# Optimization experiments

Hardware: AMD Instinct MI355X
Metric: run time of the kernel (lower is better)

## Reference

```python
import jax, jax.numpy as jnp
import numpy as np

N_NODES = 100000
N_EDGES = 500000
HEADS = 4
HID = 64
N_GRAPHS = 512
EPS_SM = 1e-8
EPS_BN = 1e-5


def setup_inputs() -> dict:
    key = jax.random.key(0)
    ks = jax.random.split(key, 8)
    x = jax.random.normal(ks[0], (N_NODES, HID), dtype=jnp.float32)
    edge_index = jax.random.randint(ks[1], (2, N_EDGES), 0, N_NODES, dtype=jnp.int64)
    batch = jnp.sort(jax.random.randint(ks[2], (N_NODES,), 0, N_GRAPHS, dtype=jnp.int64))
    Ws = jax.random.normal(ks[3], (3, HEADS * HID, HID), dtype=jnp.float32) * 0.08
    att_src = jax.random.normal(ks[4], (3, HEADS, HID), dtype=jnp.float32) * 0.1
    att_dst = jax.random.normal(ks[5], (3, HEADS, HID), dtype=jnp.float32) * 0.1
    bn_gamma = jnp.ones((2, HID), dtype=jnp.float32)
    bn_beta = jnp.zeros((2, HID), dtype=jnp.float32)
    bn_mean = jnp.zeros((2, HID), dtype=jnp.float32)
    bn_var = jnp.ones((2, HID), dtype=jnp.float32)
    fc_w = jax.random.normal(ks[6], (2, HID), dtype=jnp.float32) * 0.1
    fc_b = jnp.zeros((2,), dtype=jnp.float32)
    return {"x": x, "edge_index": edge_index, "batch": batch, "Ws": Ws,
            "att_src": att_src, "att_dst": att_dst, "bn_gamma": bn_gamma,
            "bn_beta": bn_beta, "bn_mean": bn_mean, "bn_var": bn_var,
            "fc_w": fc_w, "fc_b": fc_b}


def gat_layer(x, row, col, W, a_src, a_dst):
    # x: [N, F] -> h: [N, H, C]
    n = x.shape[0]
    h = (x @ W.T).reshape(n, HEADS, HID)
    a_s = jnp.sum(h * a_src[None], axis=-1)          # [N, H]
    a_d = jnp.sum(h * a_dst[None], axis=-1)          # [N, H]
    e = a_s[row] + a_d[col]                          # [E, H]
    e = jnp.where(e >= 0, e, 0.2 * e)                # LeakyReLU(0.2)
    # segment softmax over destination node (col)
    e_max = jax.ops.segment_max(e, col, num_segments=n)  # [N, H]
    p = jnp.exp(e - e_max[col])
    p_sum = jax.ops.segment_sum(p, col, num_segments=n)
    alpha = p / (p_sum[col] + EPS_SM)                # [E, H]
    msg = h[row] * alpha[:, :, None]                 # [E, H, C]
    out = jax.ops.segment_sum(msg, col, num_segments=n)  # [N, H, C]
    return out.mean(axis=1)                          # [N, C]


def reference(x, edge_index, batch, Ws, att_src, att_dst,
              bn_gamma, bn_beta, bn_mean, bn_var, fc_w, fc_b):
    row, col = edge_index[0], edge_index[1]
    h = x
    for i in range(2):  # first num_layers-1 layers: conv -> BN(eval) -> ReLU
        h = gat_layer(h, row, col, Ws[i], att_src[i], att_dst[i])
        h = (h - bn_mean[i]) * jax.lax.rsqrt(bn_var[i] + EPS_BN) * bn_gamma[i] + bn_beta[i]
        h = jax.nn.relu(h)
        # dropout is inactive in eval mode
    h = gat_layer(h, row, col, Ws[2], att_src[2], att_dst[2])
    # global mean pool over graphs in batch
    sums = jax.ops.segment_sum(h, batch, num_segments=N_GRAPHS)          # [G, C]
    cnts = jax.ops.segment_sum(jnp.ones_like(batch, dtype=h.dtype), batch,
                               num_segments=N_GRAPHS)                    # [G]
    pooled = sums / jnp.maximum(cnts, 1.0)[:, None]
    return pooled @ fc_w.T + fc_b                                        # [G, out]
```

## Files before the change

### kernel.cpp

```cpp
#include <hip/hip_runtime.h>


#define THREADS 256
#define LDP 36

__global__ __launch_bounds__(THREADS) void k_prep(
    const float* __restrict__ Ws, const float* __restrict__ att_src,
    const float* __restrict__ att_dst, float* __restrict__ fold)
{
    int idx = blockIdx.x * THREADS + threadIdx.x;
    if (idx >= 3 * 2 * 4 * 64) return;
    int k = idx & 63, head = (idx >> 6) & 3, sd = (idx >> 8) & 1, l = idx >> 9;
    const float* att = (sd ? att_dst : att_src) + l * 256 + head * 64;
    const float* Wb  = Ws + (size_t)l * 16384 + (size_t)head * 64 * 64;
    float s = 0.f;
    #pragma unroll
    for (int c = 0; c < 64; ++c) s = fmaf(Wb[(size_t)c * 64 + k], att[c], s);
    fold[((l * 2 + sd) * 4 + head) * 64 + k] = s;
}

__global__ __launch_bounds__(THREADS) void k_gemm(
    const float* __restrict__ x, const float* __restrict__ W,
    float* __restrict__ h, int n)
{
    __shared__ float xs[128][LDP];
    __shared__ float ws[128][LDP];
    const int tid  = threadIdx.x;
    const int tc   = tid & 15;
    const int tr   = tid >> 4;
    const int row0 = blockIdx.x * 128;
    const int col0 = blockIdx.y * 128;

    float acc[8][8];
    #pragma unroll
    for (int i = 0; i < 8; ++i)
        #pragma unroll
        for (int j = 0; j < 8; ++j) acc[i][j] = 0.f;

    for (int ks2 = 0; ks2 < 2; ++ks2) {
        #pragma unroll
        for (int i = 0; i < 4; ++i) {
            int flat4 = i * 256 + tid;
            int r  = flat4 >> 3;
            int c4 = flat4 & 7;
            int gr = row0 + r;
            float4 v = make_float4(0.f, 0.f, 0.f, 0.f);
            if (gr < n) v = *(const float4*)(x + (size_t)gr * 64 + ks2 * 32 + c4 * 4);
            *(float4*)&xs[r][c4 * 4] = v;
            int gp = col0 + r;
            int pr = (gp & 3) * 64 + (gp >> 2);
            float4 wv = *(const float4*)(W + (size_t)pr * 64 + ks2 * 32 + c4 * 4);
            *(float4*)&ws[r][c4 * 4] = wv;
        }
        __syncthreads();

        #pragma unroll 1
        for (int ks = 0; ks < 8; ++ks) {
            float4 xr[8];
            #pragma unroll
            for (int i = 0; i < 8; ++i) xr[i] = *(const float4*)&xs[tr + 16 * i][ks * 4];
            #pragma unroll
            for (int j = 0; j < 8; ++j) {
                float4 w4 = *(const float4*)&ws[tc + 16 * j][ks * 4];
                #pragma unroll
                for (int i = 0; i < 8; ++i) {
                    acc[i][j] = fmaf(xr[i].x, w4.x, acc[i][j]);
                    acc[i][j] = fmaf(xr[i].y, w4.y, acc[i][j]);
                    acc[i][j] = fmaf(xr[i].z, w4.z, acc[i][j]);
                    acc[i][j] = fmaf(xr[i].w, w4.w, acc[i][j]);
                }
            }
        }
        __syncthreads();
    }

    #pragma unroll
    for (int i = 0; i < 8; ++i) {
        int r = row0 + tr + 16 * i;
        if (r < n) {
            float* hp = h + (size_t)r * 256 + col0 + tc;
            #pragma unroll
            for (int j = 0; j < 8; ++j) hp[16 * j] = acc[i][j];
        }
    }
}

__global__ __launch_bounds__(THREADS) void k_att(
    const float* __restrict__ x, const float* __restrict__ fold_l,
    float* __restrict__ a_s, float* __restrict__ a_d, int n)
{
    int wid  = (blockIdx.x * THREADS + threadIdx.x) >> 6;
    int lane = threadIdx.x & 63;
    if (wid >= n) return;
    int vec = lane >> 3, ch = lane & 7;
    const float* xp = x + (size_t)wid * 64 + ch * 8;
    float4 v0 = *(const float4*)xp;
    float4 v1 = *(const float4*)(xp + 4);
    const float* fp = fold_l + vec * 64 + ch * 8;
    float acc = v0.x * fp[0] + v0.y * fp[1] + v0.z * fp[2] + v0.w * fp[3]
              + v1.x * fp[4] + v1.y * fp[5] + v1.z * fp[6] + v1.w * fp[7];
    acc += __shfl_xor(acc, 1, 64);
    acc += __shfl_xor(acc, 2, 64);
    acc += __shfl_xor(acc, 4, 64);
    if (ch == 0) {
        if (vec < 4) a_s[(size_t)wid * 4 + vec] = acc;
        else         a_d[(size_t)wid * 4 + (vec - 4)] = acc;
    }
}

__global__ __launch_bounds__(THREADS) void k_hist(
    const int* __restrict__ col, int* __restrict__ hist, int E)
{
    int e = blockIdx.x * THREADS + threadIdx.x;
    if (e < E) atomicAdd(hist + col[e], 1);
}

__global__ __launch_bounds__(THREADS) void k_scan1(
    const int* __restrict__ hist, int* __restrict__ offs, int* __restrict__ partials, int n)
{
    __shared__ int buf0[256], buf1[256];
    int tid = threadIdx.x;
    int i = blockIdx.x * 256 + tid;
    int v = (i < n) ? hist[i] : 0;
    buf0[tid] = v;
    __syncthreads();
    int* src = buf0; int* dst = buf1;
    #pragma unroll
    for (int off = 1; off < 256; off <<= 1) {
        int t = src[tid];
        if (tid >= off) t += src[tid - off];
        dst[tid] = t;
        __syncthreads();
        int* tmp = src; src = dst; dst = tmp;
    }
    if (i < n) offs[i] = src[tid] - v;
    if (tid == 255) partials[blockIdx.x] = src[255];
}

__global__ __launch_bounds__(512) void k_scan2(int* __restrict__ partials, int nb)
{
    __shared__ int buf0[512], buf1[512];
    int tid = threadIdx.x;
    int v = (tid < nb) ? partials[tid] : 0;
    buf0[tid] = v;
    __syncthreads();
    int* src = buf0; int* dst = buf1;
    #pragma unroll
    for (int off = 1; off < 512; off <<= 1) {
        int t = src[tid];
        if (tid >= off) t += src[tid - off];
        dst[tid] = t;
        __syncthreads();
        int* tmp = src; src = dst; dst = tmp;
    }
    if (tid < nb) partials[tid] = src[tid] - v;
}

__global__ __launch_bounds__(THREADS) void k_scan3(
    int* __restrict__ offs, const int* __restrict__ partials, int n)
{
    int i = blockIdx.x * THREADS + threadIdx.x;
    if (i < n) offs[i] += partials[i >> 8];
}

__global__ __launch_bounds__(THREADS) void k_scatter(
    const int* __restrict__ row, const int* __restrict__ col,
    const int* __restrict__ offs, int* __restrict__ tmpc,
    int* __restrict__ rs, int E)
{
    int e = blockIdx.x * THREADS + threadIdx.x;
    if (e >= E) return;
    int c = col[e];
    int pos = offs[c] + atomicAdd(tmpc + c, 1);
    rs[pos] = row[e];
}

__global__ __launch_bounds__(THREADS) void k_alpha(
    const int* __restrict__ rs, const int* __restrict__ offs, const int* __restrict__ deg,
    const float* __restrict__ a_s, const float* __restrict__ a_d,
    float* __restrict__ alpha, float* __restrict__ psum, int n)
{
    int v = blockIdx.x * THREADS + threadIdx.x;
    if (v >= n) return;
    const int start = offs[v];
    const int d     = deg[v];
    const float4 ad = *(const float4*)(a_d + (size_t)v * 4);

    float m0 = -1e30f, m1 = -1e30f, m2 = -1e30f, m3 = -1e30f;
    for (int i = 0; i < d; ++i) {
        int r = rs[start + i];
        float4 as = *(const float4*)(a_s + (size_t)r * 4);
        float v0 = as.x + ad.x, v1 = as.y + ad.y, v2 = as.z + ad.z, v3 = as.w + ad.w;
        v0 = v0 >= 0.f ? v0 : 0.2f * v0;
        v1 = v1 >= 0.f ? v1 : 0.2f * v1;
        v2 = v2 >= 0.f ? v2 : 0.2f * v2;
        v3 = v3 >= 0.f ? v3 : 0.2f * v3;
        *(float4*)(alpha + (size_t)(start + i) * 4) = make_float4(v0, v1, v2, v3);
        m0 = fmaxf(m0, v0); m1 = fmaxf(m1, v1); m2 = fmaxf(m2, v2); m3 = fmaxf(m3, v3);
    }
    float ps0 = 0.f, ps1 = 0.f, ps2 = 0.f, ps3 = 0.f;
    for (int i = 0; i < d; ++i) {
        float4 s = *(const float4*)(alpha + (size_t)(start + i) * 4);
        float p0 = __expf(s.x - m0), p1 = __expf(s.y - m1);
        float p2 = __expf(s.z - m2), p3 = __expf(s.w - m3);
        ps0 += p0; ps1 += p1; ps2 += p2; ps3 += p3;
        *(float4*)(alpha + (size_t)(start + i) * 4) = make_float4(p0, p1, p2, p3);
    }
    *(float4*)(psum + (size_t)v * 4) = make_float4(ps0, ps1, ps2, ps3);
}

__global__ __launch_bounds__(THREADS) void k_gat(
    const int* __restrict__ rs, const int* __restrict__ offs, const int* __restrict__ deg,
    const float* __restrict__ alpha, const float* __restrict__ psum,
    const float* __restrict__ h,
    const float* __restrict__ bng, const float* __restrict__ bnb,
    const float* __restrict__ bnm, const float* __restrict__ bnv, int use_bn,
    float* __restrict__ out, int n)
{
    int wid  = (blockIdx.x * THREADS + threadIdx.x) >> 6;
    int lane = threadIdx.x & 63;
    if (wid >= n) return;
    const int start = offs[wid];
    const int d     = deg[wid];
    float4 ps = *(const float4*)(psum + (size_t)wid * 4);
    const float i0 = 0.25f / (ps.x + 1e-8f), i1 = 0.25f / (ps.y + 1e-8f);
    const float i2 = 0.25f / (ps.z + 1e-8f), i3 = 0.25f / (ps.w + 1e-8f);

    float acc = 0.f;
    for (int i = 0; i < d; ++i) {
        int r = rs[start + i];
        float4 a = *(const float4*)(alpha + (size_t)(start + i) * 4);
        float4 v = *(const float4*)(h + (size_t)r * 256 + lane * 4);
        acc = fmaf(a.x * i0, v.x, acc);
        acc = fmaf(a.y * i1, v.y, acc);
        acc = fmaf(a.z * i2, v.z, acc);
        acc = fmaf(a.w * i3, v.w, acc);
    }
    if (use_bn) {
        float scale = bng[lane] * rsqrtf(bnv[lane] + 1e-5f);
        float shift = bnb[lane] - bnm[lane] * scale;
        acc = fmaxf(fmaf(acc, scale, shift), 0.f);
    }
    out[(size_t)wid * 64 + lane] = acc;
}

#define POOL_CHUNK 32
__global__ __launch_bounds__(THREADS) void k_pool(
    const float* __restrict__ xf, const int* __restrict__ batch,
    float* __restrict__ sums, float* __restrict__ cnt, int n)
{
    int wid  = (blockIdx.x * THREADS + threadIdx.x) >> 6;
    int lane = threadIdx.x & 63;
    int n0 = wid * POOL_CHUNK;
    if (n0 >= n) return;
    int n1 = min(n0 + POOL_CHUNK, n);
    int g = batch[n0];
    float acc = 0.f, c = 0.f;
    for (int i = n0; i < n1; ++i) {
        int gi = batch[i];
        if (gi != g) {
            atomicAdd(sums + (size_t)g * 64 + lane, acc);
            if (lane == 0) atomicAdd(cnt + g, c);
            g = gi; acc = 0.f; c = 0.f;
        }
        acc += xf[(size_t)i * 64 + lane];
        c += 1.f;
    }
    atomicAdd(sums + (size_t)g * 64 + lane, acc);
    if (lane == 0) atomicAdd(cnt + g, c);
}

__global__ __launch_bounds__(THREADS) void k_fc(
    const float* __restrict__ sums, const float* __restrict__ cnt,
    const float* __restrict__ fw, const float* __restrict__ fb,
    float* __restrict__ out, int G)
{
    int g = blockIdx.x * THREADS + threadIdx.x;
    if (g >= G) return;
    float cdiv = fmaxf(cnt[g], 1.f);
    float o0 = fb[0], o1 = fb[1];
    for (int k = 0; k < 64; ++k) {
        float p = sums[(size_t)g * 64 + k] / cdiv;
        o0 = fmaf(p, fw[k], o0);
        o1 = fmaf(p, fw[64 + k], o1);
    }
    out[(size_t)g * 2 + 0] = o0;
    out[(size_t)g * 2 + 1] = o1;
}

static inline size_t align256(size_t x) { return (x + 255) & ~(size_t)255; }

extern "C" void kernel_launch(void* const* d_in, const int* in_sizes, int n_in,
                              void* d_out, int out_size, void* d_ws, size_t ws_size,
                              hipStream_t stream)
{
    const float* x        = (const float*)d_in[0];
    const int*   eidx     = (const int*)d_in[1];
    const int*   batch    = (const int*)d_in[2];
    const float* Ws       = (const float*)d_in[3];
    const float* att_src  = (const float*)d_in[4];
    const float* att_dst  = (const float*)d_in[5];
    const float* bn_gamma = (const float*)d_in[6];
    const float* bn_beta  = (const float*)d_in[7];
    const float* bn_mean  = (const float*)d_in[8];
    const float* bn_var   = (const float*)d_in[9];
    const float* fc_w     = (const float*)d_in[10];
    const float* fc_b     = (const float*)d_in[11];

    const int N = in_sizes[0] / 64;
    const int E = in_sizes[1] / 2;
    const int G = 512;
    const int* row = eidx;
    const int* col = eidx + E;

    char* p = (char*)d_ws;
    float* h     = (float*)p; p += align256((size_t)N * 256 * 4);
    float* a_s   = (float*)p; p += align256((size_t)N * 4 * 4);
    float* a_d   = (float*)p; p += align256((size_t)N * 4 * 4);
    float* psum  = (float*)p; p += align256((size_t)N * 4 * 4);
    float* xb0   = (float*)p; p += align256((size_t)N * 64 * 4);
    float* xb1   = (float*)p; p += align256((size_t)N * 64 * 4);
    int*   hist  = (int*)p;   p += align256((size_t)N * 4);
    int*   offs  = (int*)p;   p += align256((size_t)N * 4);
    int*   tmpc  = (int*)p;   p += align256((size_t)N * 4);
    int*   part  = (int*)p;   p += align256((size_t)1024 * 4);
    int*   rs    = (int*)p;   p += align256((size_t)E * 4);
    float* alpha = (float*)p; p += align256((size_t)E * 4 * 4);
    float* fold  = (float*)p; p += align256((size_t)1536 * 4);
    float* sums  = (float*)p; p += align256((size_t)G * 64 * 4);
    float* cnt   = (float*)p; p += align256((size_t)G * 4);
    (void)ws_size; (void)n_in; (void)out_size;

    const int nb = (N + 255) / 256;

    k_prep<<<6, THREADS, 0, stream>>>(Ws, att_src, att_dst, fold);
    hipMemsetAsync(hist, 0, (size_t)N * 4, stream);
    hipMemsetAsync(tmpc, 0, (size_t)N * 4, stream);
    k_hist<<<(E + THREADS - 1) / THREADS, THREADS, 0, stream>>>(col, hist, E);
    k_scan1<<<nb, THREADS, 0, stream>>>(hist, offs, part, N);
    k_scan2<<<1, 512, 0, stream>>>(part, nb);
    k_scan3<<<nb, THREADS, 0, stream>>>(offs, part, N);
    k_scatter<<<(E + THREADS - 1) / THREADS, THREADS, 0, stream>>>(row, col, offs, tmpc, rs, E);

    const float* xin = x;
    for (int l = 0; l < 3; ++l) {
        float* xout = (l == 1) ? xb1 : xb0;
        dim3 ggrid((N + 127) / 128, 2);
        k_gemm<<<ggrid, THREADS, 0, stream>>>(xin, Ws + (size_t)l * 16384, h, N);
        k_att<<<((size_t)N * 64 + THREADS - 1) / THREADS, THREADS, 0, stream>>>(
            xin, fold + (size_t)l * 512, a_s, a_d, N);
        k_alpha<<<(N + THREADS - 1) / THREADS, THREADS, 0, stream>>>(
            rs, offs, hist, a_s, a_d, alpha, psum, N);
        k_gat<<<((size_t)N * 64 + THREADS - 1) / THREADS, THREADS, 0, stream>>>(
            rs, offs, hist, alpha, psum, h,
            bn_gamma + l * 64, bn_beta + l * 64, bn_mean + l * 64, bn_var + l * 64,
            (l < 2) ? 1 : 0, xout, N);
        xin = xout;
    }

    hipMemsetAsync(sums, 0, (size_t)G * 64 * 4, stream);
    hipMemsetAsync(cnt, 0, (size_t)G * 4, stream);
    int pool_waves = (N + POOL_CHUNK - 1) / POOL_CHUNK;
    k_pool<<<((size_t)pool_waves * 64 + THREADS - 1) / THREADS, THREADS, 0, stream>>>(
        xin, batch, sums, cnt, N);
    k_fc<<<(G + THREADS - 1) / THREADS, THREADS, 0, stream>>>(
        sums, cnt, fc_w, fc_b, (float*)d_out, G);
}
```

Baseline: 611.2 us.

## Fuse attention logits into GEMM and parallelize segment softmax per edge

Attention score projections a_s and a_d are now computed inside the GEMM kernel's y=0 blocks from the already staged shared-memory x tile, which removes the separate k_att pass. The per-node serial softmax kernel is replaced by two edge-parallel kernels. One computes the LeakyReLU scores and takes the per-node max with order-preserving unsigned atomicMax. The other exponentiates and accumulates psum with float atomicAdd. This trades the load imbalance of the thread-per-node loop for atomic contention, extra index arrays (dsb, pose), and per-layer memsets.

```diff
diff --git a/kernel.cpp b/kernel.cpp
--- a/kernel.cpp
+++ b/kernel.cpp
@@ -3,6 +3,15 @@
 
 #define THREADS 256
 #define LDP 36
+#define SFP 68
+
+__device__ __forceinline__ unsigned fkey(float f) {
+    unsigned u = __float_as_uint(f);
+    return (u & 0x80000000u) ? ~u : (u | 0x80000000u);
+}
+__device__ __forceinline__ float funkey(unsigned u) {
+    return __uint_as_float((u & 0x80000000u) ? (u & 0x7FFFFFFFu) : ~u);
+}
 
 __global__ __launch_bounds__(THREADS) void k_prep(
     const float* __restrict__ Ws, const float* __restrict__ att_src,
@@ -21,21 +30,33 @@
 
 __global__ __launch_bounds__(THREADS) void k_gemm(
     const float* __restrict__ x, const float* __restrict__ W,
-    float* __restrict__ h, int n)
+    const float* __restrict__ fold_l,
+    float* __restrict__ h, float* __restrict__ a_s, float* __restrict__ a_d, int n)
 {
     __shared__ float xs[128][LDP];
     __shared__ float ws[128][LDP];
+    __shared__ float sf[8 * SFP];
     const int tid  = threadIdx.x;
     const int tc   = tid & 15;
     const int tr   = tid >> 4;
     const int row0 = blockIdx.x * 128;
     const int col0 = blockIdx.y * 128;
+    const bool gy0 = (blockIdx.y == 0);
+
+    if (gy0) {
+        #pragma unroll
+        for (int j = 0; j < 2; ++j) {
+            int idx = j * 256 + tid;
+            sf[(idx >> 6) * SFP + (idx & 63)] = fold_l[idx];
+        }
+    }
 
     float acc[8][8];
     #pragma unroll
     for (int i = 0; i < 8; ++i)
         #pragma unroll
         for (int j = 0; j < 8; ++j) acc[i][j] = 0.f;
+    float pa[4] = {0.f, 0.f, 0.f, 0.f};
 
     for (int ks2 = 0; ks2 < 2; ++ks2) {
         #pragma unroll
@@ -71,6 +92,18 @@
                 }
             }
         }
+        if (gy0) {
+            const int vec = tid & 7;
+            #pragma unroll
+            for (int j = 0; j < 4; ++j) {
+                int row = j * 32 + (tid >> 3);
+                float s = 0.f;
+                #pragma unroll
+                for (int k = 0; k < 32; ++k)
+                    s = fmaf(xs[row][k], sf[vec * SFP + ks2 * 32 + k], s);
+                pa[j] += s;
+            }
+        }
         __syncthreads();
     }
 
@@ -83,28 +116,16 @@
             for (int j = 0; j < 8; ++j) hp[16 * j] = acc[i][j];
         }
     }
-}
-
-__global__ __launch_bounds__(THREADS) void k_att(
-    const float* __restrict__ x, const float* __restrict__ fold_l,
-    float* __restrict__ a_s, float* __restrict__ a_d, int n)
-{
-    int wid  = (blockIdx.x * THREADS + threadIdx.x) >> 6;
-    int lane = threadIdx.x & 63;
-    if (wid >= n) return;
-    int vec = lane >> 3, ch = lane & 7;
-    const float* xp = x + (size_t)wid * 64 + ch * 8;
-    float4 v0 = *(const float4*)xp;
-    float4 v1 = *(const float4*)(xp + 4);
-    const float* fp = fold_l + vec * 64 + ch * 8;
-    float acc = v0.x * fp[0] + v0.y * fp[1] + v0.z * fp[2] + v0.w * fp[3]
-              + v1.x * fp[4] + v1.y * fp[5] + v1.z * fp[6] + v1.w * fp[7];
-    acc += __shfl_xor(acc, 1, 64);
-    acc += __shfl_xor(acc, 2, 64);
-    acc += __shfl_xor(acc, 4, 64);
-    if (ch == 0) {
-        if (vec < 4) a_s[(size_t)wid * 4 + vec] = acc;
-        else         a_d[(size_t)wid * 4 + (vec - 4)] = acc;
+    if (gy0) {
+        const int vec = tid & 7;
+        #pragma unroll
+        for (int j = 0; j < 4; ++j) {
+            int rr = row0 + j * 32 + (tid >> 3);
+            if (rr < n) {
+                if (vec < 4) a_s[(size_t)rr * 4 + vec] = pa[j];
+                else         a_d[(size_t)rr * 4 + (vec - 4)] = pa[j];
+            }
+        }
     }
 }
 
@@ -166,47 +187,61 @@
 __global__ __launch_bounds__(THREADS) void k_scatter(
     const int* __restrict__ row, const int* __restrict__ col,
     const int* __restrict__ offs, int* __restrict__ tmpc,
-    int* __restrict__ rs, int E)
+    int* __restrict__ rs, int* __restrict__ ds, int* __restrict__ pose, int E)
 {
     int e = blockIdx.x * THREADS + threadIdx.x;
     if (e >= E) return;
     int c = col[e];
     int pos = offs[c] + atomicAdd(tmpc + c, 1);
     rs[pos] = row[e];
-}
-
-__global__ __launch_bounds__(THREADS) void k_alpha(
-    const int* __restrict__ rs, const int* __restrict__ offs, const int* __restrict__ deg,
+    ds[pos] = c;
+    pose[e] = pos;
+}
+
+__global__ __launch_bounds__(THREADS) void k_score(
+    const int* __restrict__ row, const int* __restrict__ col,
+    const int* __restrict__ pose,
     const float* __restrict__ a_s, const float* __restrict__ a_d,
-    float* __restrict__ alpha, float* __restrict__ psum, int n)
-{
-    int v = blockIdx.x * THREADS + threadIdx.x;
-    if (v >= n) return;
-    const int start = offs[v];
-    const int d     = deg[v];
-    const float4 ad = *(const float4*)(a_d + (size_t)v * 4);
-
-    float m0 = -1e30f, m1 = -1e30f, m2 = -1e30f, m3 = -1e30f;
-    for (int i = 0; i < d; ++i) {
-        int r = rs[start + i];
-        float4 as = *(const float4*)(a_s + (size_t)r * 4);
-        float v0 = as.x + ad.x, v1 = as.y + ad.y, v2 = as.z + ad.z, v3 = as.w + ad.w;
-        v0 = v0 >= 0.f ? v0 : 0.2f * v0;
-        v1 = v1 >= 0.f ? v1 : 0.2f * v1;
-        v2 = v2 >= 0.f ? v2 : 0.2f * v2;
-        v3 = v3 >= 0.f ? v3 : 0.2f * v3;
-        *(float4*)(alpha + (size_t)(start + i) * 4) = make_float4(v0, v1, v2, v3);
-        m0 = fmaxf(m0, v0); m1 = fmaxf(m1, v1); m2 = fmaxf(m2, v2); m3 = fmaxf(m3, v3);
-    }
-    float ps0 = 0.f, ps1 = 0.f, ps2 = 0.f, ps3 = 0.f;
-    for (int i = 0; i < d; ++i) {
-        float4 s = *(const float4*)(alpha + (size_t)(start + i) * 4);
-        float p0 = __expf(s.x - m0), p1 = __expf(s.y - m1);
-        float p2 = __expf(s.z - m2), p3 = __expf(s.w - m3);
-        ps0 += p0; ps1 += p1; ps2 += p2; ps3 += p3;
-        *(float4*)(alpha + (size_t)(start + i) * 4) = make_float4(p0, p1, p2, p3);
-    }
-    *(float4*)(psum + (size_t)v * 4) = make_float4(ps0, ps1, ps2, ps3);
+    float* __restrict__ palpha, unsigned* __restrict__ emax, int E)
+{
+    int e = blockIdx.x * THREADS + threadIdx.x;
+    if (e >= E) return;
+    int r = row[e], c = col[e];
+    float4 as = *(const float4*)(a_s + (size_t)r * 4);
+    float4 ad = *(const float4*)(a_d + (size_t)c * 4);
+    float v0 = as.x + ad.x, v1 = as.y + ad.y, v2 = as.z + ad.z, v3 = as.w + ad.w;
+    v0 = v0 >= 0.f ? v0 : 0.2f * v0;
+    v1 = v1 >= 0.f ? v1 : 0.2f * v1;
+    v2 = v2 >= 0.f ? v2 : 0.2f * v2;
+    v3 = v3 >= 0.f ? v3 : 0.2f * v3;
+    int pos = pose[e];
+    *(float4*)(palpha + (size_t)pos * 4) = make_float4(v0, v1, v2, v3);
+    unsigned* mp = emax + (size_t)c * 4;
+    atomicMax(mp + 0, fkey(v0));
+    atomicMax(mp + 1, fkey(v1));
+    atomicMax(mp + 2, fkey(v2));
+    atomicMax(mp + 3, fkey(v3));
+}
+
+__global__ __launch_bounds__(THREADS) void k_exp(
+    const int* __restrict__ ds, float* __restrict__ palpha,
+    const unsigned* __restrict__ emax, float* __restrict__ psum, int E)
+{
+    int i = blockIdx.x * THREADS + threadIdx.x;
+    if (i >= E) return;
+    int c = ds[i];
+    float4 s = *(const float4*)(palpha + (size_t)i * 4);
+    const unsigned* mp = emax + (size_t)c * 4;
+    float p0 = __expf(s.x - funkey(mp[0]));
+    float p1 = __expf(s.y - funkey(mp[1]));
+    float p2 = __expf(s.z - funkey(mp[2]));
+    float p3 = __expf(s.w - funkey(mp[3]));
+    *(float4*)(palpha + (size_t)i * 4) = make_float4(p0, p1, p2, p3);
+    float* pp = psum + (size_t)c * 4;
+    atomicAdd(pp + 0, p0);
+    atomicAdd(pp + 1, p1);
+    atomicAdd(pp + 2, p2);
+    atomicAdd(pp + 3, p3);
 }
 
 __global__ __launch_bounds__(THREADS) void k_gat(
@@ -314,43 +349,48 @@
     const int* col = eidx + E;
 
     char* p = (char*)d_ws;
-    float* h     = (float*)p; p += align256((size_t)N * 256 * 4);
-    float* a_s   = (float*)p; p += align256((size_t)N * 4 * 4);
-    float* a_d   = (float*)p; p += align256((size_t)N * 4 * 4);
-    float* psum  = (float*)p; p += align256((size_t)N * 4 * 4);
-    float* xb0   = (float*)p; p += align256((size_t)N * 64 * 4);
-    float* xb1   = (float*)p; p += align256((size_t)N * 64 * 4);
-    int*   hist  = (int*)p;   p += align256((size_t)N * 4);
-    int*   offs  = (int*)p;   p += align256((size_t)N * 4);
-    int*   tmpc  = (int*)p;   p += align256((size_t)N * 4);
-    int*   part  = (int*)p;   p += align256((size_t)1024 * 4);
-    int*   rs    = (int*)p;   p += align256((size_t)E * 4);
-    float* alpha = (float*)p; p += align256((size_t)E * 4 * 4);
-    float* fold  = (float*)p; p += align256((size_t)1536 * 4);
-    float* sums  = (float*)p; p += align256((size_t)G * 64 * 4);
-    float* cnt   = (float*)p; p += align256((size_t)G * 4);
+    float*    h     = (float*)p;    p += align256((size_t)N * 256 * 4);
+    float*    a_s   = (float*)p;    p += align256((size_t)N * 4 * 4);
+    float*    a_d   = (float*)p;    p += align256((size_t)N * 4 * 4);
+    float*    psum  = (float*)p;    p += align256((size_t)N * 4 * 4);
+    unsigned* emax  = (unsigned*)p; p += align256((size_t)N * 4 * 4);
+    float*    xb0   = (float*)p;    p += align256((size_t)N * 64 * 4);
+    float*    xb1   = (float*)p;    p += align256((size_t)N * 64 * 4);
+    int*      hist  = (int*)p;      p += align256((size_t)N * 4);
+    int*      offs  = (int*)p;      p += align256((size_t)N * 4);
+    int*      tmpc  = (int*)p;      p += align256((size_t)N * 4);
+    int*      part  = (int*)p;      p += align256((size_t)1024 * 4);
+    int*      rs    = (int*)p;      p += align256((size_t)E * 4);
+    int*      dsb   = (int*)p;      p += align256((size_t)E * 4);
+    int*      pose  = (int*)p;      p += align256((size_t)E * 4);
+    float*    alpha = (float*)p;    p += align256((size_t)E * 4 * 4);
+    float*    fold  = (float*)p;    p += align256((size_t)1536 * 4);
+    float*    sums  = (float*)p;    p += align256((size_t)G * 64 * 4);
+    float*    cnt   = (float*)p;    p += align256((size_t)G * 4);
     (void)ws_size; (void)n_in; (void)out_size;
 
     const int nb = (N + 255) / 256;
+    const int eb = (E + THREADS - 1) / THREADS;
 
     k_prep<<<6, THREADS, 0, stream>>>(Ws, att_src, att_dst, fold);
     hipMemsetAsync(hist, 0, (size_t)N * 4, stream);
     hipMemsetAsync(tmpc, 0, (size_t)N * 4, stream);
-    k_hist<<<(E + THREADS - 1) / THREADS, THREADS, 0, stream>>>(col, hist, E);
+    k_hist<<<eb, THREADS, 0, stream>>>(col, hist, E);
     k_scan1<<<nb, THREADS, 0, stream>>>(hist, offs, part, N);
     k_scan2<<<1, 512, 0, stream>>>(part, nb);
     k_scan3<<<nb, THREADS, 0, stream>>>(offs, part, N);
-    k_scatter<<<(E + THREADS - 1) / THREADS, THREADS, 0, stream>>>(row, col, offs, tmpc, rs, E);
+    k_scatter<<<eb, THREADS, 0, stream>>>(row, col, offs, tmpc, rs, dsb, pose, E);
 
     const float* xin = x;
     for (int l = 0; l < 3; ++l) {
         float* xout = (l == 1) ? xb1 : xb0;
+        hipMemsetAsync(emax, 0, (size_t)N * 4 * 4, stream);
+        hipMemsetAsync(psum, 0, (size_t)N * 4 * 4, stream);
         dim3 ggrid((N + 127) / 128, 2);
-        k_gemm<<<ggrid, THREADS, 0, stream>>>(xin, Ws + (size_t)l * 16384, h, N);
-        k_att<<<((size_t)N * 64 + THREADS - 1) / THREADS, THREADS, 0, stream>>>(
-            xin, fold + (size_t)l * 512, a_s, a_d, N);
-        k_alpha<<<(N + THREADS - 1) / THREADS, THREADS, 0, stream>>>(
-            rs, offs, hist, a_s, a_d, alpha, psum, N);
+        k_gemm<<<ggrid, THREADS, 0, stream>>>(
+            xin, Ws + (size_t)l * 16384, fold + (size_t)l * 512, h, a_s, a_d, N);
+        k_score<<<eb, THREADS, 0, stream>>>(row, col, pose, a_s, a_d, alpha, emax, E);
+        k_exp<<<eb, THREADS, 0, stream>>>(dsb, alpha, emax, psum, E);
         k_gat<<<((size_t)N * 64 + THREADS - 1) / THREADS, THREADS, 0, stream>>>(
             rs, offs, hist, alpha, psum, h,
             bn_gamma + l * 64, bn_beta + l * 64, bn_mean + l * 64, bn_var + l * 64,
```

After: 1.127 ms. 84.4% more time.

## Fuse attention projections into GEMM and compute edge scores edge-parallel

Applied to the files above, without the earlier changes.

The per-node attention dot products (a_s, a_d) are now computed inside the GEMM kernel from the x tile already in shared memory, so the separate k_att launch and its extra pass over x go away. Edge scores are computed by a new edge-parallel kernel that writes each LeakyReLU score straight to its CSR slot, using a position array recorded during the scatter. The per-node softmax kernel then only reads contiguous scores. The cost is one more E-sized int buffer, random writes into alpha, and extra shared-memory work in the blockIdx.y==0 GEMM blocks, which makes those blocks heavier than the others.

```diff
diff --git a/kernel.cpp b/kernel.cpp
--- a/kernel.cpp
+++ b/kernel.cpp
@@ -3,6 +3,7 @@
 
 #define THREADS 256
 #define LDP 36
+#define SFP 68
 
 __global__ __launch_bounds__(THREADS) void k_prep(
     const float* __restrict__ Ws, const float* __restrict__ att_src,
@@ -21,21 +22,33 @@
 
 __global__ __launch_bounds__(THREADS) void k_gemm(
     const float* __restrict__ x, const float* __restrict__ W,
-    float* __restrict__ h, int n)
+    const float* __restrict__ fold_l,
+    float* __restrict__ h, float* __restrict__ a_s, float* __restrict__ a_d, int n)
 {
     __shared__ float xs[128][LDP];
     __shared__ float ws[128][LDP];
+    __shared__ float sf[8 * SFP];
     const int tid  = threadIdx.x;
     const int tc   = tid & 15;
     const int tr   = tid >> 4;
     const int row0 = blockIdx.x * 128;
     const int col0 = blockIdx.y * 128;
+    const bool gy0 = (blockIdx.y == 0);
+
+    if (gy0) {
+        #pragma unroll
+        for (int j = 0; j < 2; ++j) {
+            int idx = j * 256 + tid;
+            sf[(idx >> 6) * SFP + (idx & 63)] = fold_l[idx];
+        }
+    }
 
     float acc[8][8];
     #pragma unroll
     for (int i = 0; i < 8; ++i)
         #pragma unroll
         for (int j = 0; j < 8; ++j) acc[i][j] = 0.f;
+    float pa[4] = {0.f, 0.f, 0.f, 0.f};
 
     for (int ks2 = 0; ks2 < 2; ++ks2) {
         #pragma unroll
@@ -71,6 +84,18 @@
                 }
             }
         }
+        if (gy0) {
+            const int vec = tid & 7;
+            #pragma unroll
+            for (int j = 0; j < 4; ++j) {
+                int row = j * 32 + (tid >> 3);
+                float s = 0.f;
+                #pragma unroll
+                for (int k = 0; k < 32; ++k)
+                    s = fmaf(xs[row][k], sf[vec * SFP + ks2 * 32 + k], s);
+                pa[j] += s;
+            }
+        }
         __syncthreads();
     }
 
@@ -83,28 +108,16 @@
             for (int j = 0; j < 8; ++j) hp[16 * j] = acc[i][j];
         }
     }
-}
-
-__global__ __launch_bounds__(THREADS) void k_att(
-    const float* __restrict__ x, const float* __restrict__ fold_l,
-    float* __restrict__ a_s, float* __restrict__ a_d, int n)
-{
-    int wid  = (blockIdx.x * THREADS + threadIdx.x) >> 6;
-    int lane = threadIdx.x & 63;
-    if (wid >= n) return;
-    int vec = lane >> 3, ch = lane & 7;
-    const float* xp = x + (size_t)wid * 64 + ch * 8;
-    float4 v0 = *(const float4*)xp;
-    float4 v1 = *(const float4*)(xp + 4);
-    const float* fp = fold_l + vec * 64 + ch * 8;
-    float acc = v0.x * fp[0] + v0.y * fp[1] + v0.z * fp[2] + v0.w * fp[3]
-              + v1.x * fp[4] + v1.y * fp[5] + v1.z * fp[6] + v1.w * fp[7];
-    acc += __shfl_xor(acc, 1, 64);
-    acc += __shfl_xor(acc, 2, 64);
-    acc += __shfl_xor(acc, 4, 64);
-    if (ch == 0) {
-        if (vec < 4) a_s[(size_t)wid * 4 + vec] = acc;
-        else         a_d[(size_t)wid * 4 + (vec - 4)] = acc;
+    if (gy0) {
+        const int vec = tid & 7;
+        #pragma unroll
+        for (int j = 0; j < 4; ++j) {
+            int rr = row0 + j * 32 + (tid >> 3);
+            if (rr < n) {
+                if (vec < 4) a_s[(size_t)rr * 4 + vec] = pa[j];
+                else         a_d[(size_t)rr * 4 + (vec - 4)] = pa[j];
+            }
+        }
     }
 }
 
@@ -166,37 +179,48 @@
 __global__ __launch_bounds__(THREADS) void k_scatter(
     const int* __restrict__ row, const int* __restrict__ col,
     const int* __restrict__ offs, int* __restrict__ tmpc,
-    int* __restrict__ rs, int E)
+    int* __restrict__ rs, int* __restrict__ pose, int E)
 {
     int e = blockIdx.x * THREADS + threadIdx.x;
     if (e >= E) return;
     int c = col[e];
     int pos = offs[c] + atomicAdd(tmpc + c, 1);
     rs[pos] = row[e];
-}
-
-__global__ __launch_bounds__(THREADS) void k_alpha(
-    const int* __restrict__ rs, const int* __restrict__ offs, const int* __restrict__ deg,
+    pose[e] = pos;
+}
+
+__global__ __launch_bounds__(THREADS) void k_score_ns(
+    const int* __restrict__ row, const int* __restrict__ col,
+    const int* __restrict__ pose,
     const float* __restrict__ a_s, const float* __restrict__ a_d,
+    float* __restrict__ alpha, int E)
+{
+    int e = blockIdx.x * THREADS + threadIdx.x;
+    if (e >= E) return;
+    int r = row[e], c = col[e];
+    float4 as = *(const float4*)(a_s + (size_t)r * 4);
+    float4 ad = *(const float4*)(a_d + (size_t)c * 4);
+    float v0 = as.x + ad.x, v1 = as.y + ad.y, v2 = as.z + ad.z, v3 = as.w + ad.w;
+    v0 = v0 >= 0.f ? v0 : 0.2f * v0;
+    v1 = v1 >= 0.f ? v1 : 0.2f * v1;
+    v2 = v2 >= 0.f ? v2 : 0.2f * v2;
+    v3 = v3 >= 0.f ? v3 : 0.2f * v3;
+    *(float4*)(alpha + (size_t)pose[e] * 4) = make_float4(v0, v1, v2, v3);
+}
+
+__global__ __launch_bounds__(THREADS) void k_alpha2(
+    const int* __restrict__ offs, const int* __restrict__ deg,
     float* __restrict__ alpha, float* __restrict__ psum, int n)
 {
     int v = blockIdx.x * THREADS + threadIdx.x;
     if (v >= n) return;
     const int start = offs[v];
     const int d     = deg[v];
-    const float4 ad = *(const float4*)(a_d + (size_t)v * 4);
-
     float m0 = -1e30f, m1 = -1e30f, m2 = -1e30f, m3 = -1e30f;
     for (int i = 0; i < d; ++i) {
-        int r = rs[start + i];
-        float4 as = *(const float4*)(a_s + (size_t)r * 4);
-        float v0 = as.x + ad.x, v1 = as.y + ad.y, v2 = as.z + ad.z, v3 = as.w + ad.w;
-        v0 = v0 >= 0.f ? v0 : 0.2f * v0;
-        v1 = v1 >= 0.f ? v1 : 0.2f * v1;
-        v2 = v2 >= 0.f ? v2 : 0.2f * v2;
-        v3 = v3 >= 0.f ? v3 : 0.2f * v3;
-        *(float4*)(alpha + (size_t)(start + i) * 4) = make_float4(v0, v1, v2, v3);
-        m0 = fmaxf(m0, v0); m1 = fmaxf(m1, v1); m2 = fmaxf(m2, v2); m3 = fmaxf(m3, v3);
+        float4 s = *(const float4*)(alpha + (size_t)(start + i) * 4);
+        m0 = fmaxf(m0, s.x); m1 = fmaxf(m1, s.y);
+        m2 = fmaxf(m2, s.z); m3 = fmaxf(m3, s.w);
     }
     float ps0 = 0.f, ps1 = 0.f, ps2 = 0.f, ps3 = 0.f;
     for (int i = 0; i < d; ++i) {
@@ -325,6 +349,7 @@
     int*   tmpc  = (int*)p;   p += align256((size_t)N * 4);
     int*   part  = (int*)p;   p += align256((size_t)1024 * 4);
     int*   rs    = (int*)p;   p += align256((size_t)E * 4);
+    int*   pose  = (int*)p;   p += align256((size_t)E * 4);
     float* alpha = (float*)p; p += align256((size_t)E * 4 * 4);
     float* fold  = (float*)p; p += align256((size_t)1536 * 4);
     float* sums  = (float*)p; p += align256((size_t)G * 64 * 4);
@@ -332,25 +357,25 @@
     (void)ws_size; (void)n_in; (void)out_size;
 
     const int nb = (N + 255) / 256;
+    const int eb = (E + THREADS - 1) / THREADS;
 
     k_prep<<<6, THREADS, 0, stream>>>(Ws, att_src, att_dst, fold);
     hipMemsetAsync(hist, 0, (size_t)N * 4, stream);
     hipMemsetAsync(tmpc, 0, (size_t)N * 4, stream);
-    k_hist<<<(E + THREADS - 1) / THREADS, THREADS, 0, stream>>>(col, hist, E);
+    k_hist<<<eb, THREADS, 0, stream>>>(col, hist, E);
     k_scan1<<<nb, THREADS, 0, stream>>>(hist, offs, part, N);
     k_scan2<<<1, 512, 0, stream>>>(part, nb);
     k_scan3<<<nb, THREADS, 0, stream>>>(offs, part, N);
-    k_scatter<<<(E + THREADS - 1) / THREADS, THREADS, 0, stream>>>(row, col, offs, tmpc, rs, E);
+    k_scatter<<<eb, THREADS, 0, stream>>>(row, col, offs, tmpc, rs, pose, E);
 
     const float* xin = x;
     for (int l = 0; l < 3; ++l) {
         float* xout = (l == 1) ? xb1 : xb0;
         dim3 ggrid((N + 127) / 128, 2);
-        k_gemm<<<ggrid, THREADS, 0, stream>>>(xin, Ws + (size_t)l * 16384, h, N);
-        k_att<<<((size_t)N * 64 + THREADS - 1) / THREADS, THREADS, 0, stream>>>(
-            xin, fold + (size_t)l * 512, a_s, a_d, N);
-        k_alpha<<<(N + THREADS - 1) / THREADS, THREADS, 0, stream>>>(
-            rs, offs, hist, a_s, a_d, alpha, psum, N);
+        k_gemm<<<ggrid, THREADS, 0, stream>>>(
+            xin, Ws + (size_t)l * 16384, fold + (size_t)l * 512, h, a_s, a_d, N);
+        k_score_ns<<<eb, THREADS, 0, stream>>>(row, col, pose, a_s, a_d, alpha, E);
+        k_alpha2<<<nb, THREADS, 0, stream>>>(offs, hist, alpha, psum, N);
         k_gat<<<((size_t)N * 64 + THREADS - 1) / THREADS, THREADS, 0, stream>>>(
             rs, offs, hist, alpha, psum, h,
             bn_gamma + l * 64, bn_beta + l * 64, bn_mean + l * 64, bn_var + l * 64,
```

Result: faster. 594.7 us (-2.7%).
